# Kernel tuning notes

Measured on AMD Instinct MI355X. Metric: run time of the kernel, lower is better.

Reference implementation:

```python
import jax, jax.numpy as jnp
import numpy as np

# Hardcoded 6-node part graph from the module (src, dst) pairs; PyG flows src->dst.
_EDGES = np.array([[0,1],[0,2],[0,3],[0,4],[0,5],[1,2],[1,3],[1,4],[1,5],[2,3],[2,4],[3,5],[4,5],[1,0],[2,0],[3,0],[4,0],[5,0],[2,1],[3,1],[4,1],[5,1],[3,2],[4,2],[5,3],[5,4]], dtype=np.int32)
SRC = jnp.asarray(_EDGES[:, 0])
DST = jnp.asarray(_EDGES[:, 1])
NUM_NODES = 6


def setup_inputs() -> dict:
    key = jax.random.key(0)
    k0, k1, k2 = jax.random.split(key, 3)
    C, B = 128, 32768
    x = jax.random.normal(k0, (NUM_NODES, B, C), dtype=jnp.float32)
    # SAGEConv weights: lin_l (aggregated neighbors, carries bias) and lin_r (root)
    W_l = jax.random.normal(k1, (2 * C, C), dtype=jnp.float32) / np.sqrt(C).astype(np.float32)
    W_r = jax.random.normal(k2, (2 * C, C), dtype=jnp.float32) / np.sqrt(C).astype(np.float32)
    b = jnp.zeros((2 * C,), dtype=jnp.float32)
    return {"x": x, "W_l": W_l, "W_r": W_r, "b": b}


def reference(x, W_l, W_r, b):
    # x: [N=6, B, C]
    # mean aggregation of source features at each destination node
    msg = x[SRC]                                                  # [E, B, C]
    agg = jax.ops.segment_sum(msg, DST, num_segments=NUM_NODES)   # [N, B, C]
    deg = jax.ops.segment_sum(jnp.ones_like(DST, dtype=x.dtype), DST, num_segments=NUM_NODES)
    agg = agg / deg[:, None, None]
    # SAGEConv: lin_l(agg) + lin_r(x), bias in lin_l
    y = jnp.einsum('nbc,oc->nbo', agg, W_l) + b + jnp.einsum('nbc,oc->nbo', x, W_r)
    y = jax.nn.gelu(y, approximate=False)                         # torch F.gelu = exact erf
    # Python cat-loop over nodes == concatenate the 6 node slices along features
    N, B, O = y.shape
    return jnp.transpose(y, (1, 0, 2)).reshape(B, N * O)          # [B, 6*2C]
```

## Files before the change

### kernel.cpp

```cpp
#include <hip/hip_runtime.h>
#include <hip/hip_bf16.h>

#define NB 32768
#define CD 128
#define NNODES 6
#define OUTW 1536
#define KW 256
#define GPB 8
#define NBLK (NB / 16 / GPB)

typedef __attribute__((ext_vector_type(8))) short short8;
typedef __attribute__((ext_vector_type(4))) short s16x4;
typedef __attribute__((ext_vector_type(4))) float f32x4;

static __device__ __forceinline__ short f2bf(float f) {
    union { __bf16 b; short s; } u;
    u.b = (__bf16)f;
    return u.s;
}

static __device__ __forceinline__ short8 pack8(f32x4 a, f32x4 b) {
    short8 p;
    #pragma unroll
    for (int j = 0; j < 4; ++j) { p[j] = f2bf(a[j]); p[4 + j] = f2bf(b[j]); }
    return p;
}

static __device__ __forceinline__ s16x4 pack4(f32x4 a) {
    s16x4 p;
    #pragma unroll
    for (int j = 0; j < 4; ++j) p[j] = f2bf(a[j]);
    return p;
}

__global__ void prep_w(const float* __restrict__ Wl, const float* __restrict__ Wr,
                       short* __restrict__ Wb) {
    const int i = (blockIdx.x * 256 + threadIdx.x) * 8;
    const int o = i >> 8;
    const int k = i & 255;
    const float* src = (k < 128) ? (Wl + o * CD + k) : (Wr + o * CD + (k - 128));
    *(short8*)(Wb + i) = pack8(*(const f32x4*)src, *(const f32x4*)(src + 4));
}

#define LIDX(p, r, k) ((((p) << 11) + ((r) << 7) + (k)) ^ (((r) & 7) << 3))

__global__ __launch_bounds__(512, 2)
void sage_v9(const float* __restrict__ x, const short* __restrict__ Wb,
             const float* __restrict__ bias, float* __restrict__ out) {
    __shared__ __align__(16) float raw[2][NNODES * 16 * 128];
    __shared__ __align__(16) short A[10 * 16 * 128];

    const int t = threadIdx.x;
    const int r = t >> 5;
    const int c = t & 31;
    const int lane = t & 63;
    const int wv = t >> 6;
    const int lo = lane & 15;
    const int hi = lane >> 4;
    const int obase = wv * 32;
    const size_t rg0 = (size_t)blockIdx.x * GPB;

    auto stage = [&](int buf, size_t rg) {
        const float* gp = x + (rg * 16 + r) * CD + c * 4;
        #pragma unroll
        for (int s = 0; s < NNODES; ++s) {
            __builtin_amdgcn_global_load_lds(
                (const __attribute__((address_space(1))) void*)(gp + (size_t)s * (NB * CD)),
                (__attribute__((address_space(3))) void*)&raw[buf][s * 2048 + wv * 256],
                16, 0, 0);
        }
    };

    auto convert = [&](int buf) {
        const float* rb = &raw[buf][0];
        const int base = r * 128 + c * 4;
        f32x4 v0 = *(const f32x4*)&rb[0 * 2048 + base];
        f32x4 v1 = *(const f32x4*)&rb[1 * 2048 + base];
        f32x4 v2 = *(const f32x4*)&rb[2 * 2048 + base];
        f32x4 v3 = *(const f32x4*)&rb[3 * 2048 + base];
        f32x4 v4 = *(const f32x4*)&rb[4 * 2048 + base];
        f32x4 v5 = *(const f32x4*)&rb[5 * 2048 + base];
        f32x4 S01 = v0 + v1, S25 = v2 + v5, S34 = v3 + v4;
        f32x4 T = S01 + S25 + S34;
        const int k = c * 4;
        *(s16x4*)&A[LIDX(0, r, k)] = pack4((T - v0) * 0.2f);
        *(s16x4*)&A[LIDX(1, r, k)] = pack4((T - v1) * 0.2f);
        *(s16x4*)&A[LIDX(2, r, k)] = pack4((S01 + S34) * 0.25f);
        *(s16x4*)&A[LIDX(3, r, k)] = pack4((S01 + S25) * 0.25f);
        *(s16x4*)&A[LIDX(4, r, k)] = pack4(v0);
        *(s16x4*)&A[LIDX(5, r, k)] = pack4(v1);
        *(s16x4*)&A[LIDX(6, r, k)] = pack4(v2);
        *(s16x4*)&A[LIDX(7, r, k)] = pack4(v3);
        *(s16x4*)&A[LIDX(8, r, k)] = pack4(v4);
        *(s16x4*)&A[LIDX(9, r, k)] = pack4(v5);
    };

    stage(0, rg0);
    __syncthreads();
    convert(0);
    __syncthreads();

    #pragma unroll 1
    for (int it = 0; it < GPB; ++it) {
        if (it + 1 < GPB) stage((it + 1) & 1, rg0 + it + 1);

        f32x4 acc[NNODES][2];
        #pragma unroll
        for (int n = 0; n < NNODES; ++n)
            #pragma unroll
            for (int i = 0; i < 2; ++i) acc[n][i] = (f32x4){0.f, 0.f, 0.f, 0.f};

        #pragma unroll
        for (int m = 0; m < 4; ++m) {
            const int kk = m * 32 + hi * 8;
            short8 fg0  = *(const short8*)&A[LIDX(0, lo, kk)];
            short8 fg1  = *(const short8*)&A[LIDX(1, lo, kk)];
            short8 fg25 = *(const short8*)&A[LIDX(2, lo, kk)];
            short8 fg34 = *(const short8*)&A[LIDX(3, lo, kk)];
            short8 fx0 = *(const short8*)&A[LIDX(4, lo, kk)];
            short8 fx1 = *(const short8*)&A[LIDX(5, lo, kk)];
            short8 fx2 = *(const short8*)&A[LIDX(6, lo, kk)];
            short8 fx3 = *(const short8*)&A[LIDX(7, lo, kk)];
            short8 fx4 = *(const short8*)&A[LIDX(8, lo, kk)];
            short8 fx5 = *(const short8*)&A[LIDX(9, lo, kk)];
            #pragma unroll
            for (int i = 0; i < 2; ++i) {
                const int o = obase + i * 16 + lo;
                short8 wa = *(const short8*)&Wb[o * KW + kk];
                short8 wx = *(const short8*)&Wb[o * KW + 128 + kk];
                acc[0][i] = __builtin_amdgcn_mfma_f32_16x16x32_bf16(wa, fg0,  acc[0][i], 0, 0, 0);
                acc[1][i] = __builtin_amdgcn_mfma_f32_16x16x32_bf16(wa, fg1,  acc[1][i], 0, 0, 0);
                acc[2][i] = __builtin_amdgcn_mfma_f32_16x16x32_bf16(wa, fg25, acc[2][i], 0, 0, 0);
                acc[3][i] = __builtin_amdgcn_mfma_f32_16x16x32_bf16(wa, fg34, acc[3][i], 0, 0, 0);
                acc[4][i] = __builtin_amdgcn_mfma_f32_16x16x32_bf16(wa, fg34, acc[4][i], 0, 0, 0);
                acc[5][i] = __builtin_amdgcn_mfma_f32_16x16x32_bf16(wa, fg25, acc[5][i], 0, 0, 0);
                acc[0][i] = __builtin_amdgcn_mfma_f32_16x16x32_bf16(wx, fx0, acc[0][i], 0, 0, 0);
                acc[1][i] = __builtin_amdgcn_mfma_f32_16x16x32_bf16(wx, fx1, acc[1][i], 0, 0, 0);
                acc[2][i] = __builtin_amdgcn_mfma_f32_16x16x32_bf16(wx, fx2, acc[2][i], 0, 0, 0);
                acc[3][i] = __builtin_amdgcn_mfma_f32_16x16x32_bf16(wx, fx3, acc[3][i], 0, 0, 0);
                acc[4][i] = __builtin_amdgcn_mfma_f32_16x16x32_bf16(wx, fx4, acc[4][i], 0, 0, 0);
                acc[5][i] = __builtin_amdgcn_mfma_f32_16x16x32_bf16(wx, fx5, acc[5][i], 0, 0, 0);
            }
        }

        const size_t orow = (rg0 + it) * 16 + lo;
        #pragma unroll
        for (int n = 0; n < NNODES; ++n) {
            #pragma unroll
            for (int i = 0; i < 2; ++i) {
                const int ocol = obase + i * 16 + hi * 4;
                f32x4 v = acc[n][i] + *(const f32x4*)&bias[ocol];
                f32x4 g;
                #pragma unroll
                for (int j = 0; j < 4; ++j) {
                    const float s = v[j] * (0.7978845608f + 0.0356774081f * v[j] * v[j]);
                    const float rr = __builtin_amdgcn_exp2f(-2.885390082f * s);
                    g[j] = v[j] * __builtin_amdgcn_rcpf(1.0f + rr);
                }
                *(f32x4*)&out[orow * OUTW + n * 256 + ocol] = g;
            }
        }

        __syncthreads();
        if (it + 1 < GPB) {
            convert((it + 1) & 1);
            __syncthreads();
        }
    }
}

extern "C" void kernel_launch(void* const* d_in, const int* in_sizes, int n_in,
                              void* d_out, int out_size, void* d_ws, size_t ws_size,
                              hipStream_t stream) {
    const float* x  = (const float*)d_in[0];
    const float* Wl = (const float*)d_in[1];
    const float* Wr = (const float*)d_in[2];
    const float* b  = (const float*)d_in[3];
    float* out = (float*)d_out;
    short* Wb = (short*)d_ws;

    prep_w<<<dim3(32), dim3(256), 0, stream>>>(Wl, Wr, Wb);
    sage_v9<<<dim3(NBLK), dim3(512), 0, stream>>>(x, Wb, b, out);
}
```

Measured before the change: 92.21 us.

## Split per-node MFMA into node pairs and overlap last store with convert

The six-node accumulator block is replaced by three passes over node pairs, each computing and storing two nodes before moving on. This cuts live accumulator registers so the 2-blocks-per-CU launch bound is easier to meet without spills. The last pair's GELU and store now run after the barrier, alongside the conversion of the next tile. Bias is hoisted into registers once per block. The cost is that weight fragments are reloaded three times per iteration instead of once.

```diff
diff --git a/kernel.cpp b/kernel.cpp
--- a/kernel.cpp
+++ b/kernel.cpp
@@ -45,8 +45,8 @@
 #define LIDX(p, r, k) ((((p) << 11) + ((r) << 7) + (k)) ^ (((r) & 7) << 3))
 
 __global__ __launch_bounds__(512, 2)
-void sage_v9(const float* __restrict__ x, const short* __restrict__ Wb,
-             const float* __restrict__ bias, float* __restrict__ out) {
+void sage_v11(const float* __restrict__ x, const short* __restrict__ Wb,
+              const float* __restrict__ bias, float* __restrict__ out) {
     __shared__ __align__(16) float raw[2][NNODES * 16 * 128];
     __shared__ __align__(16) short A[10 * 16 * 128];
 
@@ -59,6 +59,11 @@
     const int hi = lane >> 4;
     const int obase = wv * 32;
     const size_t rg0 = (size_t)blockIdx.x * GPB;
+
+    f32x4 bias4[2];
+    #pragma unroll
+    for (int i = 0; i < 2; ++i)
+        bias4[i] = *(const f32x4*)&bias[obase + i * 16 + hi * 4];
 
     auto stage = [&](int buf, size_t rg) {
         const float* gp = x + (rg * 16 + r) * CD + c * 4;
@@ -95,6 +100,51 @@
         *(s16x4*)&A[LIDX(9, r, k)] = pack4(v5);
     };
 
+    auto pairMFMA = [&](int pa0, int pa1, int px0, int px1, f32x4 acc[2][2]) {
+        #pragma unroll
+        for (int n = 0; n < 2; ++n)
+            #pragma unroll
+            for (int i = 0; i < 2; ++i) acc[n][i] = (f32x4){0.f, 0.f, 0.f, 0.f};
+        #pragma unroll
+        for (int m = 0; m < 4; ++m) {
+            const int kk = m * 32 + hi * 8;
+            short8 fa0 = *(const short8*)&A[LIDX(pa0, lo, kk)];
+            short8 fa1 = *(const short8*)&A[LIDX(pa1, lo, kk)];
+            short8 fx0 = *(const short8*)&A[LIDX(px0, lo, kk)];
+            short8 fx1 = *(const short8*)&A[LIDX(px1, lo, kk)];
+            #pragma unroll
+            for (int i = 0; i < 2; ++i) {
+                const int o = obase + i * 16 + lo;
+                short8 wa = *(const short8*)&Wb[o * KW + kk];
+                short8 wx = *(const short8*)&Wb[o * KW + 128 + kk];
+                acc[0][i] = __builtin_amdgcn_mfma_f32_16x16x32_bf16(wa, fa0, acc[0][i], 0, 0, 0);
+                acc[1][i] = __builtin_amdgcn_mfma_f32_16x16x32_bf16(wa, fa1, acc[1][i], 0, 0, 0);
+                acc[0][i] = __builtin_amdgcn_mfma_f32_16x16x32_bf16(wx, fx0, acc[0][i], 0, 0, 0);
+                acc[1][i] = __builtin_amdgcn_mfma_f32_16x16x32_bf16(wx, fx1, acc[1][i], 0, 0, 0);
+            }
+        }
+    };
+
+    auto storePair = [&](int n0, int n1, f32x4 acc[2][2], size_t orow) {
+        #pragma unroll
+        for (int w = 0; w < 2; ++w) {
+            const int node = w ? n1 : n0;
+            #pragma unroll
+            for (int i = 0; i < 2; ++i) {
+                const int ocol = obase + i * 16 + hi * 4;
+                f32x4 v = acc[w][i] + bias4[i];
+                f32x4 g;
+                #pragma unroll
+                for (int j = 0; j < 4; ++j) {
+                    const float s = v[j] * (0.7978845608f + 0.0356774081f * v[j] * v[j]);
+                    const float rr = __builtin_amdgcn_exp2f(-2.885390082f * s);
+                    g[j] = v[j] * __builtin_amdgcn_rcpf(1.0f + rr);
+                }
+                *(f32x4*)&out[orow * OUTW + node * 256 + ocol] = g;
+            }
+        }
+    };
+
     stage(0, rg0);
     __syncthreads();
     convert(0);
@@ -102,70 +152,22 @@
 
     #pragma unroll 1
     for (int it = 0; it < GPB; ++it) {
-        if (it + 1 < GPB) stage((it + 1) & 1, rg0 + it + 1);
-
-        f32x4 acc[NNODES][2];
-        #pragma unroll
-        for (int n = 0; n < NNODES; ++n)
-            #pragma unroll
-            for (int i = 0; i < 2; ++i) acc[n][i] = (f32x4){0.f, 0.f, 0.f, 0.f};
-
-        #pragma unroll
-        for (int m = 0; m < 4; ++m) {
-            const int kk = m * 32 + hi * 8;
-            short8 fg0  = *(const short8*)&A[LIDX(0, lo, kk)];
-            short8 fg1  = *(const short8*)&A[LIDX(1, lo, kk)];
-            short8 fg25 = *(const short8*)&A[LIDX(2, lo, kk)];
-            short8 fg34 = *(const short8*)&A[LIDX(3, lo, kk)];
-            short8 fx0 = *(const short8*)&A[LIDX(4, lo, kk)];
-            short8 fx1 = *(const short8*)&A[LIDX(5, lo, kk)];
-            short8 fx2 = *(const short8*)&A[LIDX(6, lo, kk)];
-            short8 fx3 = *(const short8*)&A[LIDX(7, lo, kk)];
-            short8 fx4 = *(const short8*)&A[LIDX(8, lo, kk)];
-            short8 fx5 = *(const short8*)&A[LIDX(9, lo, kk)];
-            #pragma unroll
-            for (int i = 0; i < 2; ++i) {
-                const int o = obase + i * 16 + lo;
-                short8 wa = *(const short8*)&Wb[o * KW + kk];
-                short8 wx = *(const short8*)&Wb[o * KW + 128 + kk];
-                acc[0][i] = __builtin_amdgcn_mfma_f32_16x16x32_bf16(wa, fg0,  acc[0][i], 0, 0, 0);
-                acc[1][i] = __builtin_amdgcn_mfma_f32_16x16x32_bf16(wa, fg1,  acc[1][i], 0, 0, 0);
-                acc[2][i] = __builtin_amdgcn_mfma_f32_16x16x32_bf16(wa, fg25, acc[2][i], 0, 0, 0);
-                acc[3][i] = __builtin_amdgcn_mfma_f32_16x16x32_bf16(wa, fg34, acc[3][i], 0, 0, 0);
-                acc[4][i] = __builtin_amdgcn_mfma_f32_16x16x32_bf16(wa, fg34, acc[4][i], 0, 0, 0);
-                acc[5][i] = __builtin_amdgcn_mfma_f32_16x16x32_bf16(wa, fg25, acc[5][i], 0, 0, 0);
-                acc[0][i] = __builtin_amdgcn_mfma_f32_16x16x32_bf16(wx, fx0, acc[0][i], 0, 0, 0);
-                acc[1][i] = __builtin_amdgcn_mfma_f32_16x16x32_bf16(wx, fx1, acc[1][i], 0, 0, 0);
-                acc[2][i] = __builtin_amdgcn_mfma_f32_16x16x32_bf16(wx, fx2, acc[2][i], 0, 0, 0);
-                acc[3][i] = __builtin_amdgcn_mfma_f32_16x16x32_bf16(wx, fx3, acc[3][i], 0, 0, 0);
-                acc[4][i] = __builtin_amdgcn_mfma_f32_16x16x32_bf16(wx, fx4, acc[4][i], 0, 0, 0);
-                acc[5][i] = __builtin_amdgcn_mfma_f32_16x16x32_bf16(wx, fx5, acc[5][i], 0, 0, 0);
-            }
-        }
+        const bool havenext = (it + 1 < GPB);
+        if (havenext) stage((it + 1) & 1, rg0 + it + 1);
 
         const size_t orow = (rg0 + it) * 16 + lo;
-        #pragma unroll
-        for (int n = 0; n < NNODES; ++n) {
-            #pragma unroll
-            for (int i = 0; i < 2; ++i) {
-                const int ocol = obase + i * 16 + hi * 4;
-                f32x4 v = acc[n][i] + *(const f32x4*)&bias[ocol];
-                f32x4 g;
-                #pragma unroll
-                for (int j = 0; j < 4; ++j) {
-                    const float s = v[j] * (0.7978845608f + 0.0356774081f * v[j] * v[j]);
-                    const float rr = __builtin_amdgcn_exp2f(-2.885390082f * s);
-                    g[j] = v[j] * __builtin_amdgcn_rcpf(1.0f + rr);
-                }
-                *(f32x4*)&out[orow * OUTW + n * 256 + ocol] = g;
-            }
-        }
+        f32x4 acc[2][2];
+
+        pairMFMA(0, 1, 4, 5, acc);
+        storePair(0, 1, acc, orow);
+        pairMFMA(2, 2, 6, 9, acc);
+        storePair(2, 5, acc, orow);
+        pairMFMA(3, 3, 7, 8, acc);
 
         __syncthreads();
-        if (it + 1 < GPB) {
-            convert((it + 1) & 1);
-            __syncthreads();
-        }
+        storePair(3, 4, acc, orow);
+        if (havenext) convert((it + 1) & 1);
+        __syncthreads();
     }
 }
 
@@ -180,5 +182,5 @@
     short* Wb = (short*)d_ws;
 
     prep_w<<<dim3(32), dim3(256), 0, stream>>>(Wl, Wr, Wb);
-    sage_v9<<<dim3(NBLK), dim3(512), 0, stream>>>(x, Wb, b, out);
+    sage_v11<<<dim3(NBLK), dim3(512), 0, stream>>>(x, Wb, b, out);
 }
```

New measurement: 83.82 us. 1.1x faster.
